# Kernel tuning notes

Hardware: AMD Instinct MI355X
Metric: run time of the kernel (lower is better)

## Reference

```python
import jax, jax.numpy as jnp
import numpy as np

# dims: B batch, T timesteps, S sensors, O obs_dim, E obs_embed_dim, P pe_emb_dim, A inter-sensor attn dim
B, T, S, O, E, P, A, OUT = 64, 128, 64, 4, 64, 16, 10, 128


def positional_encoding(times, pe_dim):
    # standard sinusoidal PE over continuous times -> (B, T, pe_dim)
    # (sin block then cos block; mathematically same frequencies as interleaved torch version)
    freq = jnp.exp(jnp.arange(0, pe_dim, 2, dtype=jnp.float32) * (-jnp.log(10000.0) / pe_dim))
    ang = times[..., None] * freq  # (B, T, pe_dim//2)
    return jnp.concatenate([jnp.sin(ang), jnp.cos(ang)], axis=-1)


def setup_inputs() -> dict:
    key = jax.random.key(0)
    ks = jax.random.split(key, 16)
    x = jax.random.normal(ks[0], (B, T, S, O), dtype=jnp.float32)
    times = jnp.sort(jax.random.uniform(ks[1], (B, T), dtype=jnp.float32) * 100.0, axis=1)
    mask = (jax.random.uniform(ks[2], (B, T, S), dtype=jnp.float32) < 0.8).astype(jnp.float32)
    s = 0.1  # param scale (module inits near zero; use small random for a meaningful baseline)
    params = dict(
        obs_emb_weights=jax.random.normal(ks[3], (S, O, E), dtype=jnp.float32) * s,
        inter_sensor_attn_weights=jax.random.normal(ks[4], (S, A), dtype=jnp.float32) * s,
        W_recv=jax.random.normal(ks[5], (E, A + P), dtype=jnp.float32) * s,
        b_recv=jax.random.normal(ks[6], (A + P,), dtype=jnp.float32) * s,
        bidir_weights=jax.random.normal(ks[7], (S, E), dtype=jnp.float32) * s,
        W_q=jax.random.normal(ks[8], (E + P, A), dtype=jnp.float32) * s,
        b_q=jax.random.normal(ks[9], (A,), dtype=jnp.float32) * s,
        W_k=jax.random.normal(ks[10], (E + P, A), dtype=jnp.float32) * s,
        b_k=jax.random.normal(ks[11], (A,), dtype=jnp.float32) * s,
        W_s=jax.random.normal(ks[12], (T, 1), dtype=jnp.float32) * s,
        b_s=jax.random.normal(ks[13], (1,), dtype=jnp.float32) * s,
        W_emb=jax.random.normal(ks[14], (E + P, OUT), dtype=jnp.float32) * s,
        b_emb=jax.random.normal(ks[15], (OUT,), dtype=jnp.float32) * s,
    )
    return dict(x=x, times=times, mask=mask, **params)


def reference(x, times, mask, obs_emb_weights, inter_sensor_attn_weights,
              W_recv, b_recv, bidir_weights, W_q, b_q, W_k, b_k,
              W_s, b_s, W_emb, b_emb):
    b, t, s, _ = x.shape
    e = obs_emb_weights.shape[-1]
    pe_dim = W_recv.shape[1] - inter_sensor_attn_weights.shape[1]

    # per-sensor observation embedding, masked
    h = jax.nn.relu(jnp.einsum('btso,soe->btse', x, obs_emb_weights))
    h = h * mask[..., None]

    pe = positional_encoding(times, pe_dim)                      # (B,T,P)
    pe_rep = jnp.broadcast_to(pe[:, :, None, :], (b, t, s, pe_dim))

    # inter-sensor attention alpha: (B,T,S_recv,S_send)
    attn_cat = jnp.concatenate(
        [jnp.broadcast_to(inter_sensor_attn_weights[None, None], (b, t, s, inter_sensor_attn_weights.shape[1])),
         pe_rep], axis=-1)                                        # (B,T,S,A+P)
    h_map = h @ W_recv + b_recv                                   # (B,T,S,A+P)
    alpha = jax.nn.relu(jnp.einsum('btid,btjd->btij', h_map, attn_cat))

    bidir = bidir_weights @ bidir_weights.T                       # (S,S)

    def propagate(h_in, adj):
        # fused form of: (h.unsqueeze(2) * (bidir*alpha*adj)[...,None]).sum(3)
        w = bidir[None, None] * alpha * adj[:, None]              # (B,T,S,S)
        return jax.nn.relu(jnp.einsum('btij,btje->btie', w, h_in))

    adj1 = jnp.ones((b, s, s), dtype=x.dtype)
    h = propagate(h, adj1)
    adj2 = adj1 * (alpha.sum(axis=1) / mask.sum(axis=1)[..., None])  # (B,S,S)
    h = propagate(h, adj2)

    H = jnp.concatenate([h, pe_rep], axis=-1).transpose(0, 2, 1, 3)  # (B,S,T,E+P)

    # temporal self-attention
    Q = H @ W_q + b_q                                             # (B,S,T,A)
    K = H @ W_k + b_k
    scale = 1.0 / jnp.sqrt(jnp.float32(e + pe_dim))
    beta = jnp.einsum('bsta,bsua->bstu', Q, K) * scale            # (B,S,T,T)
    beta = (beta @ W_s)[..., 0] + b_s[0]                          # (B,S,T)
    beta = jax.nn.softmax(beta, axis=-1)

    out = jnp.einsum('bst,bstd->bsd', beta, H) @ W_emb + b_emb    # (B,S,OUT)
    return out
```

## Files before the change

### kernel.cpp

```cpp
#include <hip/hip_runtime.h>
#include <hip/hip_bf16.h>


typedef unsigned short u16;
typedef unsigned int u32;
typedef __attribute__((ext_vector_type(8))) short short8;
typedef __attribute__((ext_vector_type(4))) float f32x4;

#define OFF_BIDIR 131072
#define OFF_MS    135168
#define OFF_ADJ   139264
#define OFF_BRP   401408
#define OFF_ST    401424
#define BOFF_WRT  1638464u
#define BOFF_CATX 1642560u
#define BOFF_PEH  1644608u
#define BOFF_ADJS 1906752u
#define BOFF_V    2431040u
#define BOFF_HH   3479616u

__device__ __forceinline__ u16 f2bf(float f){
  __hip_bfloat16 h = __float2bfloat16(f);
  union { __hip_bfloat16 h; u16 u; } v; v.h = h; return v.u;
}
__device__ __forceinline__ u32 pk2bf(float lo, float hi){
  __hip_bfloat162 h = __float22bfloat162_rn(float2{lo, hi});
  union { __hip_bfloat162 h; u32 u; } v; v.h = h; return v.u;
}
__device__ __forceinline__ float bf2f(u16 h){
  union { u32 u; float f; } v; v.u = ((u32)h) << 16; return v.f;
}

__global__ void k_pre(const float* __restrict__ times, const float* __restrict__ mask,
                      const float* __restrict__ Wb, const float* __restrict__ Wrecv,
                      const float* __restrict__ brecv, const float* __restrict__ battn,
                      float* __restrict__ ws_f, char* __restrict__ ws_b) {
  __shared__ float peL[32][17];
  __shared__ float wpe[64][17];
  __shared__ float pm[4][64];
  const int blk = blockIdx.x, tid = threadIdx.x;
  u16* wrt  = (u16*)(ws_b + BOFF_WRT);
  u16* catx = (u16*)(ws_b + BOFF_CATX);
  u16* peh  = (u16*)(ws_b + BOFF_PEH);
  u16* vv   = (u16*)(ws_b + BOFF_V);
  float* ST = ws_f + OFF_ST;
  if (blk < 256) {
    #pragma unroll
    for (int r = 0; r < 2; ++r) {
      int id = blk * 512 + r * 256 + tid;
      int bt = id >> 4, k = id & 15;
      float tv = times[bt];
      int kk = k & 7;
      float fr = expf(-(float)kk * 1.1512925465f);
      float ang = tv * fr;
      float v = (k < 8) ? sinf(ang) : cosf(ang);
      peh[id] = f2bf(v);
      peL[r*16 + (tid >> 4)][k] = v;
    }
    #pragma unroll
    for (int q = 0; q < 4; ++q) {
      int idx = q * 256 + tid;
      wpe[idx >> 4][idx & 15] = Wrecv[(idx >> 4)*26 + 10 + (idx & 15)];
    }
    __syncthreads();
    {
      int btl = tid >> 3, e0 = (tid & 7) * 8;
      float acc[8];
      #pragma unroll
      for (int i = 0; i < 8; ++i) acc[i] = 0.f;
      #pragma unroll
      for (int k = 0; k < 16; ++k) {
        float p = peL[btl][k];
        #pragma unroll
        for (int i = 0; i < 8; ++i) acc[i] += wpe[e0 + i][k] * p;
      }
      u32* dst = (u32*)&vv[(blk*32 + btl)*64 + e0];
      #pragma unroll
      for (int p = 0; p < 4; ++p) dst[p] = pk2bf(acc[2*p], acc[2*p+1]);
      if (tid < 32) {
        float s = 0.f;
        #pragma unroll
        for (int k = 0; k < 16; ++k) s += brecv[10 + k] * peL[tid][k];
        ST[blk*32 + tid] = s;
      }
    }
  } else if (blk < 260) {
    float* bidir = ws_f + OFF_BIDIR;
    int q = blk - 256;
    for (int rr = 0; rr < 4; ++rr) {
      int idx = (q*4 + rr) * 256 + tid;
      int i = idx >> 6, j = idx & 63;
      float acc = 0.f;
      for (int e = 0; e < 64; ++e) acc += Wb[i*64+e] * Wb[j*64+e];
      bidir[idx] = acc;
    }
  } else if (blk == 260) {
    for (int r = 0; r < 8; ++r) {
      int idx = r * 256 + tid;
      int d = idx >> 6, e = idx & 63;
      wrt[idx] = (d < 26) ? f2bf(Wrecv[e*26 + d]) : (u16)0;
    }
    if (tid < 16) ws_f[OFF_BRP + tid] = (tid < 10) ? brecv[tid] : 0.f;
    #pragma unroll
    for (int i = 0; i < 4; ++i) {
      int idx = i * 256 + tid;
      int j = idx >> 4, d = idx & 15;
      catx[idx] = (d < 10) ? f2bf(battn[j*10 + d]) : ((d == 10) ? f2bf(1.f) : (u16)0);
    }
  } else {
    int b = blk - 261;
    int i = tid & 63, q = tid >> 6;
    float s = 0.f;
    for (int t = q*32; t < q*32 + 32; ++t) s += mask[(b*128 + t)*64 + i];
    pm[q][i] = s;
    __syncthreads();
    if (tid < 64)
      (ws_f + OFF_MS)[b*64 + tid] =
          1.0f / (pm[0][tid] + pm[1][tid] + pm[2][tid] + pm[3][tid]);
  }
}

__global__ __launch_bounds__(256)
void k_adj(const float* __restrict__ x, const float* __restrict__ mask,
           const float* __restrict__ Wobs, float* __restrict__ ws_f,
           const char* __restrict__ ws_b) {
  __shared__ __align__(16) u16 hA[64][72];
  __shared__ __align__(16) u16 hmA[64][24];

  const int tid = threadIdx.x;
  const int b = blockIdx.y, tc = blockIdx.x;
  const int w = tid >> 6, l = tid & 63, lr = l & 15, lq = l >> 4, kb = lq * 8;
  const u16* wrt  = (const u16*)(ws_b + BOFF_WRT);
  const u16* catx = (const u16*)(ws_b + BOFF_CATX);
  const u16* vv   = (const u16*)(ws_b + BOFF_V);
  const float* brp = ws_f + OFF_BRP;
  const float* ST = ws_f + OFF_ST;
  float* adj = ws_f + OFF_ADJ;

  const short8 z8 = (short8){0,0,0,0,0,0,0,0};
  const bool lowk = (lq < 2);
  short8 w0 = z8, w1 = z8;
  if (lr < 10) {
    const u16* wr = wrt + lr * 64;
    w0 = *(const short8*)&wr[kb];
    w1 = *(const short8*)&wr[32 + kb];
  }
  short8 bc[4];
  #pragma unroll
  for (int n = 0; n < 4; ++n)
    bc[n] = lowk ? *(const short8*)&catx[(16*n + lr)*16 + lq*8] : z8;
  float4 bv = *(const float4*)&brp[lq*4];

  f32x4 asum[4];
  #pragma unroll
  for (int n = 0; n < 4; ++n) asum[n] = (f32x4){0.f,0.f,0.f,0.f};

  const int e4 = tid & 15, sg = tid >> 4;

  for (int tt = 0; tt < 8; ++tt) {
    int t = tc * 8 + tt;
    int base = b * 128 + t;
    short8 av0 = z8, av1 = z8;
    if (lr == 10) {
      av0 = *(const short8*)&vv[base*64 + kb];
      av1 = *(const short8*)&vv[base*64 + 32 + kb];
    }
    float st = ST[base];
    {
      float4 mk4 = *(const float4*)&mask[base*64 + sg*4];
      float mks[4] = {mk4.x, mk4.y, mk4.z, mk4.w};
      #pragma unroll
      for (int si = 0; si < 4; ++si) {
        int s = sg*4 + si;
        float4 xv = *(const float4*)&x[base*256 + s*4];
        float xo[4] = {xv.x, xv.y, xv.z, xv.w};
        float ax = 0.f, ay = 0.f, az = 0.f, aw = 0.f;
        #pragma unroll
        for (int o = 0; o < 4; ++o) {
          float4 wv = *(const float4*)&Wobs[(s*4+o)*64 + e4*4];
          ax += xo[o]*wv.x; ay += xo[o]*wv.y; az += xo[o]*wv.z; aw += xo[o]*wv.w;
        }
        float mk = mks[si];
        uint2 p;
        p.x = pk2bf(fmaxf(ax,0.f)*mk, fmaxf(ay,0.f)*mk);
        p.y = pk2bf(fmaxf(az,0.f)*mk, fmaxf(aw,0.f)*mk);
        *(uint2*)&hA[s][e4*4] = p;
      }
    }
    __syncthreads();
    {
      short8 a0 = (lr < 10) ? w0 : av0;
      short8 a1 = (lr < 10) ? w1 : av1;
      f32x4 acc = (f32x4){0.f,0.f,0.f,0.f};
      short8 b0 = *(const short8*)&hA[16*w + lr][kb];
      short8 b1 = *(const short8*)&hA[16*w + lr][32 + kb];
      acc = __builtin_amdgcn_mfma_f32_16x16x32_bf16(a0, b0, acc, 0, 0, 0);
      acc = __builtin_amdgcn_mfma_f32_16x16x32_bf16(a1, b1, acc, 0, 0, 0);
      uint2 qq;
      qq.x = pk2bf(acc[0]+bv.x, acc[1]+bv.y);
      qq.y = pk2bf(acc[2]+bv.z, acc[3]+bv.w);
      *(uint2*)&hmA[16*w + lr][lq*4] = qq;
    }
    __syncthreads();
    {
      short8 am = lowk ? *(const short8*)&hmA[16*w + lr][lq*8] : z8;
      #pragma unroll
      for (int n = 0; n < 4; ++n) {
        f32x4 z = (f32x4){st, st, st, st};
        z = __builtin_amdgcn_mfma_f32_16x16x32_bf16(am, bc[n], z, 0, 0, 0);
        #pragma unroll
        for (int reg = 0; reg < 4; ++reg) asum[n][reg] += fmaxf(z[reg], 0.f);
      }
    }
    __syncthreads();
  }
  #pragma unroll
  for (int n = 0; n < 4; ++n) {
    #pragma unroll
    for (int reg = 0; reg < 4; ++reg) {
      int i = 16*w + lq*4 + reg, j = 16*n + lr;
      atomicAdd(&adj[((size_t)b << 12) + (i << 6) + j], asum[n][reg]);
    }
  }
}

__global__ __launch_bounds__(256)
void k_scale(const float* __restrict__ ws_f, char* __restrict__ ws_b) {
  const int b = blockIdx.x, tid = threadIdx.x;
  const float* adj = ws_f + OFF_ADJ + (size_t)b * 4096;
  const float* msI = ws_f + OFF_MS + b * 64;
  u16* as_ = (u16*)(ws_b + BOFF_ADJS) + (size_t)b * 4096;
  #pragma unroll
  for (int k = 0; k < 16; ++k) {
    int idx = k * 256 + tid;
    int i = idx >> 6;
    as_[idx] = f2bf(adj[idx] * msI[i]);
  }
}

__global__ __launch_bounds__(256, 4)
void k_main(const float* __restrict__ x, const float* __restrict__ mask,
            const float* __restrict__ Wobs, const float* __restrict__ ws_f,
            const char* __restrict__ ws_b, u16* __restrict__ Hh) {
  __shared__ __align__(16) char smem[36864];
  u16 (*hA)[72]  = (u16 (*)[72])(smem);
  u16 (*hT)[72]  = (u16 (*)[72])(smem + 9216);
  u16 (*wA)[72]  = (u16 (*)[72])(smem + 18432);
  u16 (*hmA)[24] = (u16 (*)[24])(smem + 27648);
  u16 (*adjS)[72]= (u16 (*)[72])(smem + 27648);

  const int tid = threadIdx.x;
  const int t = blockIdx.x, b = blockIdx.y;
  const int w = tid >> 6, l = tid & 63, lr = l & 15, lq = l >> 4, kb = lq * 8;
  const int base = b * 128 + t;
  const u16* wrt  = (const u16*)(ws_b + BOFF_WRT);
  const u16* catx = (const u16*)(ws_b + BOFF_CATX);
  const u16* vv   = (const u16*)(ws_b + BOFF_V);
  const float* bidirG = ws_f + OFF_BIDIR;
  const float* brp = ws_f + OFF_BRP;
  const int i0 = 16*w + lq*4;
  const short8 z8 = (short8){0,0,0,0,0,0,0,0};
  const bool lowk = (lq < 2);

  const uint4* ag = (const uint4*)(ws_b + BOFF_ADJS + (size_t)b * 8192);
  uint4 g0 = ag[2*tid], g1 = ag[2*tid + 1];
  short8 w0 = z8, w1 = z8;
  if (lr < 10) {
    const u16* wr = wrt + lr * 64;
    w0 = *(const short8*)&wr[kb];
    w1 = *(const short8*)&wr[32 + kb];
  }
  short8 av0 = z8, av1 = z8;
  if (lr == 10) {
    av0 = *(const short8*)&vv[base*64 + kb];
    av1 = *(const short8*)&vv[base*64 + 32 + kb];
  }
  short8 bc[4];
  #pragma unroll
  for (int n = 0; n < 4; ++n)
    bc[n] = lowk ? *(const short8*)&catx[(16*n + lr)*16 + lq*8] : z8;
  float4 bv = *(const float4*)&brp[lq*4];
  const float st = (ws_f + OFF_ST)[base];

  {
    const int e4 = tid & 15, sg = tid >> 4;
    float4 mk4 = *(const float4*)&mask[base*64 + sg*4];
    float mks[4] = {mk4.x, mk4.y, mk4.z, mk4.w};
    #pragma unroll
    for (int si = 0; si < 4; ++si) {
      int s = sg*4 + si;
      float4 xv = *(const float4*)&x[base*256 + s*4];
      float xo[4] = {xv.x, xv.y, xv.z, xv.w};
      float ax = 0.f, ay = 0.f, az = 0.f, aw = 0.f;
      #pragma unroll
      for (int o = 0; o < 4; ++o) {
        float4 wv = *(const float4*)&Wobs[(s*4+o)*64 + e4*4];
        ax += xo[o]*wv.x; ay += xo[o]*wv.y; az += xo[o]*wv.z; aw += xo[o]*wv.w;
      }
      float mk = mks[si];
      uint2 p;
      p.x = pk2bf(fmaxf(ax,0.f)*mk, fmaxf(ay,0.f)*mk);
      p.y = pk2bf(fmaxf(az,0.f)*mk, fmaxf(aw,0.f)*mk);
      *(uint2*)&hA[s][e4*4] = p;
    }
  }
  __syncthreads();

  {
    #pragma unroll
    for (int sp = 0; sp < 8; ++sp) {
      int s = w*16 + sp*2;
      *(u32*)&hT[l][s] = (u32)hA[s][l] | ((u32)hA[s+1][l] << 16);
    }
    short8 a0 = (lr < 10) ? w0 : av0;
    short8 a1 = (lr < 10) ? w1 : av1;
    f32x4 acc = (f32x4){0.f,0.f,0.f,0.f};
    short8 b0 = *(const short8*)&hA[16*w + lr][kb];
    short8 b1 = *(const short8*)&hA[16*w + lr][32 + kb];
    acc = __builtin_amdgcn_mfma_f32_16x16x32_bf16(a0, b0, acc, 0, 0, 0);
    acc = __builtin_amdgcn_mfma_f32_16x16x32_bf16(a1, b1, acc, 0, 0, 0);
    uint2 qq;
    qq.x = pk2bf(acc[0]+bv.x, acc[1]+bv.y);
    qq.y = pk2bf(acc[2]+bv.z, acc[3]+bv.w);
    *(uint2*)&hmA[16*w + lr][lq*4] = qq;
  }
  __syncthreads();

  {
    short8 am = lowk ? *(const short8*)&hmA[16*w + lr][lq*8] : z8;
    #pragma unroll
    for (int n = 0; n < 4; ++n) {
      f32x4 z = (f32x4){st, st, st, st};
      z = __builtin_amdgcn_mfma_f32_16x16x32_bf16(am, bc[n], z, 0, 0, 0);
      int j = 16*n + lr;
      #pragma unroll
      for (int reg = 0; reg < 4; ++reg) {
        float w1v = fmaxf(z[reg], 0.f) * bidirG[((i0+reg) << 6) + j];
        wA[i0 + reg][j] = f2bf(w1v);
      }
    }
  }
  __syncthreads();

  {
    int idx0 = 2*tid, idx1 = 2*tid + 1;
    *(uint4*)&adjS[idx0 >> 3][(idx0 & 7) * 8] = g0;
    *(uint4*)&adjS[idx1 >> 3][(idx1 & 7) * 8] = g1;

    short8 aw0 = *(const short8*)&wA[16*w + lr][kb];
    short8 aw1 = *(const short8*)&wA[16*w + lr][32 + kb];
    #pragma unroll
    for (int n = 0; n < 4; ++n) {
      f32x4 acc = (f32x4){0.f,0.f,0.f,0.f};
      short8 b0 = *(const short8*)&hT[16*n + lr][kb];
      short8 b1 = *(const short8*)&hT[16*n + lr][32 + kb];
      acc = __builtin_amdgcn_mfma_f32_16x16x32_bf16(aw0, b0, acc, 0, 0, 0);
      acc = __builtin_amdgcn_mfma_f32_16x16x32_bf16(aw1, b1, acc, 0, 0, 0);
      int e = 16*n + lr;
      uint2 pp;
      pp.x = pk2bf(fmaxf(acc[0],0.f), fmaxf(acc[1],0.f));
      pp.y = pk2bf(fmaxf(acc[2],0.f), fmaxf(acc[3],0.f));
      *(uint2*)&hA[e][i0] = pp;
    }
  }
  __syncthreads();

  {
    int row = 16*w + lr;
    union { short8 v; u16 h[8]; u32 u[4]; } uw0, uw1, ud0, ud1, oa, ob;
    uw0.v = *(const short8*)&wA[row][kb];
    uw1.v = *(const short8*)&wA[row][32 + kb];
    ud0.v = *(const short8*)&adjS[row][kb];
    ud1.v = *(const short8*)&adjS[row][32 + kb];
    #pragma unroll
    for (int k = 0; k < 4; ++k) {
      oa.u[k] = pk2bf(bf2f(uw0.h[2*k])*bf2f(ud0.h[2*k]),
                      bf2f(uw0.h[2*k+1])*bf2f(ud0.h[2*k+1]));
      ob.u[k] = pk2bf(bf2f(uw1.h[2*k])*bf2f(ud1.h[2*k]),
                      bf2f(uw1.h[2*k+1])*bf2f(ud1.h[2*k+1]));
    }
    short8 a20 = oa.v, a21 = ob.v;
    size_t obase = ((size_t)b * 64) * 8192 + (size_t)t * 64;
    #pragma unroll
    for (int n = 0; n < 4; ++n) {
      f32x4 acc = (f32x4){0.f,0.f,0.f,0.f};
      short8 b0 = *(const short8*)&hA[16*n + lr][kb];
      short8 b1 = *(const short8*)&hA[16*n + lr][32 + kb];
      acc = __builtin_amdgcn_mfma_f32_16x16x32_bf16(a20, b0, acc, 0, 0, 0);
      acc = __builtin_amdgcn_mfma_f32_16x16x32_bf16(a21, b1, acc, 0, 0, 0);
      int e = 16*n + lr;
      u32 p0 = pk2bf(fmaxf(acc[0],0.f), fmaxf(acc[1],0.f));
      u32 p1 = pk2bf(fmaxf(acc[2],0.f), fmaxf(acc[3],0.f));
      Hh[obase + (size_t)(i0+0) * 8192 + e] = (u16)p0;
      Hh[obase + (size_t)(i0+1) * 8192 + e] = (u16)(p0 >> 16);
      Hh[obase + (size_t)(i0+2) * 8192 + e] = (u16)p1;
      Hh[obase + (size_t)(i0+3) * 8192 + e] = (u16)(p1 >> 16);
    }
  }
}

#define HTP 82

__global__ __launch_bounds__(512)
void k_attn(const char* __restrict__ ws_b, const u16* __restrict__ Hh,
            const float* __restrict__ Wq, const float* __restrict__ bq,
            const float* __restrict__ Wk, const float* __restrict__ bk,
            const float* __restrict__ Ws, const float* __restrict__ bs,
            const float* __restrict__ Wemb, const float* __restrict__ bemb,
            float* __restrict__ out) {
  __shared__ u16 Ht[128][HTP];
  __shared__ u16 peB[128][18];
  __shared__ float wsL[128];
  __shared__ float pA[6][80];
  __shared__ float pK[8][10];
  __shared__ float qvL[80];
  __shared__ float pC[4][128];
  __shared__ float bb[128];
  __shared__ float red[4];
  __shared__ float cstL, sWL;

  const int tid = threadIdx.x;
  const int s = blockIdx.x, b = blockIdx.y;
  const float scale = 0.111803398875f;
  const u16* peh = (const u16*)(ws_b + BOFF_PEH);

  const u16* src = Hh + ((size_t)b * 64 + s) * 8192;
  #pragma unroll
  for (int r = 0; r < 2; ++r) {
    int id = r * 512 + tid;
    int tt = id >> 3, c = (id & 7) * 8;
    uint4 q = *(const uint4*)&src[tt * 64 + c];
    u32* dst = (u32*)&Ht[tt][c];
    dst[0] = q.x; dst[1] = q.y; dst[2] = q.z; dst[3] = q.w;
  }
  #pragma unroll
  for (int r = 0; r < 2; ++r) {
    int id = r * 512 + tid;
    u32 pv = ((const u32*)(peh + (size_t)b * 2048))[id];
    *(u32*)&peB[id >> 3][(id & 7) * 2] = pv;
  }
  if (tid < 128) wsL[tid] = Ws[tid];
  __syncthreads();

  if (tid < 480) {
    int d = tid % 80, c = tid / 80;
    int t0 = c * 22, t1 = (t0 + 22 > 128) ? 128 : t0 + 22;
    float a0 = 0.f, a1 = 0.f, a2 = 0.f, a3 = 0.f;
    int t = t0;
    if (d < 64) {
      for (; t + 4 <= t1; t += 4) {
        a0 += wsL[t]   * bf2f(Ht[t][d]);
        a1 += wsL[t+1] * bf2f(Ht[t+1][d]);
        a2 += wsL[t+2] * bf2f(Ht[t+2][d]);
        a3 += wsL[t+3] * bf2f(Ht[t+3][d]);
      }
      for (; t < t1; ++t) a0 += wsL[t] * bf2f(Ht[t][d]);
    } else {
      int k = d - 64;
      for (; t + 4 <= t1; t += 4) {
        a0 += wsL[t]   * bf2f(peB[t][k]);
        a1 += wsL[t+1] * bf2f(peB[t+1][k]);
        a2 += wsL[t+2] * bf2f(peB[t+2][k]);
        a3 += wsL[t+3] * bf2f(peB[t+3][k]);
      }
      for (; t < t1; ++t) a0 += wsL[t] * bf2f(peB[t][k]);
    }
    pA[c][d] = (a0 + a1) + (a2 + a3);
  } else if (tid == 480) {
    float a0 = 0.f, a1 = 0.f, a2 = 0.f, a3 = 0.f;
    for (int t = 0; t < 128; t += 4) {
      a0 += wsL[t]; a1 += wsL[t+1]; a2 += wsL[t+2]; a3 += wsL[t+3];
    }
    sWL = (a0 + a1) + (a2 + a3);
  }
  __syncthreads();

  if (tid < 80) {
    int a = tid % 10, c = tid / 10;
    float a0 = 0.f, a1 = 0.f;
    #pragma unroll
    for (int i = 0; i < 10; i += 2) {
      int d = c * 10 + i;
      float h0 = pA[0][d] + pA[1][d] + pA[2][d] + pA[3][d] + pA[4][d] + pA[5][d];
      float h1 = pA[0][d+1] + pA[1][d+1] + pA[2][d+1] + pA[3][d+1] + pA[4][d+1] + pA[5][d+1];
      a0 += h0 * Wk[d * 10 + a];
      a1 += h1 * Wk[(d+1) * 10 + a];
    }
    pK[c][a] = a0 + a1;
  }
  __syncthreads();

  if (tid <= 80) {
    float kt[10];
    #pragma unroll
    for (int a = 0; a < 10; ++a) {
      float acc = sWL * bk[a];
      #pragma unroll
      for (int c = 0; c < 8; ++c) acc += pK[c][a];
      kt[a] = acc;
    }
    if (tid < 80) {
      float a0 = 0.f, a1 = 0.f;
      #pragma unroll
      for (int a = 0; a < 10; a += 2) {
        a0 += Wq[tid * 10 + a] * kt[a];
        a1 += Wq[tid * 10 + a + 1] * kt[a + 1];
      }
      qvL[tid] = a0 + a1;
    } else {
      float cq = 0.f;
      #pragma unroll
      for (int a = 0; a < 10; ++a) cq += bq[a] * kt[a];
      cstL = scale * cq + bs[0];
    }
  }
  __syncthreads();

  {
    int t = tid & 127, q = tid >> 7;
    float a0 = 0.f, a1 = 0.f, a2 = 0.f, a3 = 0.f;
    const u32* row = (const u32*)&Ht[t][0];
    if (q == 0) {
      #pragma unroll
      for (int i = 0; i < 10; i += 2) {
        u32 p0 = row[i], p1 = row[i+1];
        a0 += bf2f((u16)p0) * qvL[2*i]   + bf2f((u16)(p0 >> 16)) * qvL[2*i+1];
        a1 += bf2f((u16)p1) * qvL[2*i+2] + bf2f((u16)(p1 >> 16)) * qvL[2*i+3];
      }
    } else if (q == 1) {
      #pragma unroll
      for (int i = 10; i < 20; i += 2) {
        u32 p0 = row[i], p1 = row[i+1];
        a0 += bf2f((u16)p0) * qvL[2*i]   + bf2f((u16)(p0 >> 16)) * qvL[2*i+1];
        a1 += bf2f((u16)p1) * qvL[2*i+2] + bf2f((u16)(p1 >> 16)) * qvL[2*i+3];
      }
    } else if (q == 2) {
      #pragma unroll
      for (int i = 20; i < 32; i += 4) {
        u32 p0 = row[i], p1 = row[i+1], p2 = row[i+2], p3 = row[i+3];
        a0 += bf2f((u16)p0) * qvL[2*i]   + bf2f((u16)(p0 >> 16)) * qvL[2*i+1];
        a1 += bf2f((u16)p1) * qvL[2*i+2] + bf2f((u16)(p1 >> 16)) * qvL[2*i+3];
        a2 += bf2f((u16)p2) * qvL[2*i+4] + bf2f((u16)(p2 >> 16)) * qvL[2*i+5];
        a3 += bf2f((u16)p3) * qvL[2*i+6] + bf2f((u16)(p3 >> 16)) * qvL[2*i+7];
      }
    } else {
      #pragma unroll
      for (int k = 0; k < 16; k += 4) {
        a0 += bf2f(peB[t][k])   * qvL[64 + k];
        a1 += bf2f(peB[t][k+1]) * qvL[65 + k];
        a2 += bf2f(peB[t][k+2]) * qvL[66 + k];
        a3 += bf2f(peB[t][k+3]) * qvL[67 + k];
      }
    }
    pC[q][t] = (a0 + a1) + (a2 + a3);
  }
  __syncthreads();

  if (tid < 128) {
    float v = scale * (pC[0][tid] + pC[1][tid] + pC[2][tid] + pC[3][tid]) + cstL;
    bb[tid] = v;
    float mm = v;
    #pragma unroll
    for (int off = 32; off; off >>= 1) mm = fmaxf(mm, __shfl_xor(mm, off));
    if ((tid & 63) == 0) red[tid >> 6] = mm;
  }
  __syncthreads();
  float mx = fmaxf(red[0], red[1]);
  if (tid < 128) {
    float ev = expf(bb[tid] - mx);
    bb[tid] = ev;
    float ss = ev;
    #pragma unroll
    for (int off = 32; off; off >>= 1) ss += __shfl_xor(ss, off);
    if ((tid & 63) == 0) red[2 + (tid >> 6)] = ss;
  }
  __syncthreads();

  if (tid < 480) {
    int d = tid % 80, c = tid / 80;
    int t0 = c * 22, t1 = (t0 + 22 > 128) ? 128 : t0 + 22;
    float a0 = 0.f, a1 = 0.f, a2 = 0.f, a3 = 0.f;
    int t = t0;
    if (d < 64) {
      for (; t + 4 <= t1; t += 4) {
        a0 += bb[t]   * bf2f(Ht[t][d]);
        a1 += bb[t+1] * bf2f(Ht[t+1][d]);
        a2 += bb[t+2] * bf2f(Ht[t+2][d]);
        a3 += bb[t+3] * bf2f(Ht[t+3][d]);
      }
      for (; t < t1; ++t) a0 += bb[t] * bf2f(Ht[t][d]);
    } else {
      int k = d - 64;
      for (; t + 4 <= t1; t += 4) {
        a0 += bb[t]   * bf2f(peB[t][k]);
        a1 += bb[t+1] * bf2f(peB[t+1][k]);
        a2 += bb[t+2] * bf2f(peB[t+2][k]);
        a3 += bb[t+3] * bf2f(peB[t+3][k]);
      }
      for (; t < t1; ++t) a0 += bb[t] * bf2f(peB[t][k]);
    }
    pA[c][d] = (a0 + a1) + (a2 + a3);
  }
  __syncthreads();

  {
    int o = tid & 127, q = tid >> 7;
    int d0 = q * 20;
    float a0 = 0.f, a1 = 0.f, a2 = 0.f, a3 = 0.f;
    #pragma unroll
    for (int i = 0; i < 20; i += 4) {
      int d = d0 + i;
      float h0 = pA[0][d]   + pA[1][d]   + pA[2][d]   + pA[3][d]   + pA[4][d]   + pA[5][d];
      float h1 = pA[0][d+1] + pA[1][d+1] + pA[2][d+1] + pA[3][d+1] + pA[4][d+1] + pA[5][d+1];
      float h2 = pA[0][d+2] + pA[1][d+2] + pA[2][d+2] + pA[3][d+2] + pA[4][d+2] + pA[5][d+2];
      float h3 = pA[0][d+3] + pA[1][d+3] + pA[2][d+3] + pA[3][d+3] + pA[4][d+3] + pA[5][d+3];
      a0 += h0 * Wemb[d * 128 + o];
      a1 += h1 * Wemb[(d+1) * 128 + o];
      a2 += h2 * Wemb[(d+2) * 128 + o];
      a3 += h3 * Wemb[(d+3) * 128 + o];
    }
    pC[q][o] = (a0 + a1) + (a2 + a3);
  }
  __syncthreads();
  if (tid < 128) {
    float rdenom = 1.0f / (red[2] + red[3]);
    out[(((size_t)b * 64 + s) << 7) + tid] =
        bemb[tid] + (pC[0][tid] + pC[1][tid] + pC[2][tid] + pC[3][tid]) * rdenom;
  }
}

extern "C" void kernel_launch(void* const* d_in, const int* in_sizes, int n_in,
                              void* d_out, int out_size, void* d_ws, size_t ws_size,
                              hipStream_t stream) {
  (void)in_sizes; (void)n_in; (void)out_size; (void)ws_size;
  const float* x     = (const float*)d_in[0];
  const float* times = (const float*)d_in[1];
  const float* mask  = (const float*)d_in[2];
  const float* Wobs  = (const float*)d_in[3];
  const float* Wattn = (const float*)d_in[4];
  const float* Wrecv = (const float*)d_in[5];
  const float* brecv = (const float*)d_in[6];
  const float* Wb    = (const float*)d_in[7];
  const float* Wq    = (const float*)d_in[8];
  const float* bq    = (const float*)d_in[9];
  const float* Wk    = (const float*)d_in[10];
  const float* bk    = (const float*)d_in[11];
  const float* Ws    = (const float*)d_in[12];
  const float* bs    = (const float*)d_in[13];
  const float* Wemb  = (const float*)d_in[14];
  const float* bemb  = (const float*)d_in[15];
  float* out = (float*)d_out;
  float* ws_f = (float*)d_ws;
  char* ws_b = (char*)d_ws;
  u16* Hh = (u16*)(ws_b + BOFF_HH);

  hipMemsetAsync(ws_b + (size_t)OFF_ADJ * 4, 0, (size_t)64 * 64 * 64 * 4, stream);
  k_pre<<<325, 256, 0, stream>>>(times, mask, Wb, Wrecv, brecv, Wattn, ws_f, ws_b);
  k_adj<<<dim3(16, 64), 256, 0, stream>>>(x, mask, Wobs, ws_f, ws_b);
  k_scale<<<64, 256, 0, stream>>>(ws_f, ws_b);
  k_main<<<dim3(128, 64), 256, 0, stream>>>(x, mask, Wobs, ws_f, ws_b, Hh);
  k_attn<<<dim3(64, 64), 512, 0, stream>>>(ws_b, Hh, Wq, bq, Wk, bk, Ws, bs, Wemb, bemb, out);
}
```

Measured before the change: 149.9 us.

## Store h and first-hop weights from k_adj instead of recomputing in k_main

k_adj now writes the transposed masked observation embedding and the bidir-scaled alpha weights to global workspace for every (b,t), and k_main loads them instead of recomputing the embedding, the receiver projection and alpha. This removes a duplicated compute pass and two block barriers in k_main, at the cost of roughly 130 MB of extra global writes and reads. The ADJ memset is also folded into extra k_pre blocks, which saves one launch.

```diff
diff --git a/kernel.cpp b/kernel.cpp
--- a/kernel.cpp
+++ b/kernel.cpp
@@ -17,7 +17,9 @@
 #define BOFF_PEH  1644608u
 #define BOFF_ADJS 1906752u
 #define BOFF_V    2431040u
-#define BOFF_HH   3479616u
+#define BOFF_W1   3479616u
+#define BOFF_HT   70588480u
+#define BOFF_HH   137697344u
 
 __device__ __forceinline__ u16 f2bf(float f){
   __hip_bfloat16 h = __float2bfloat16(f);
@@ -107,7 +109,7 @@
       int j = idx >> 4, d = idx & 15;
       catx[idx] = (d < 10) ? f2bf(battn[j*10 + d]) : ((d == 10) ? f2bf(1.f) : (u16)0);
     }
-  } else {
+  } else if (blk < 325) {
     int b = blk - 261;
     int i = tid & 63, q = tid >> 6;
     float s = 0.f;
@@ -117,24 +119,32 @@
     if (tid < 64)
       (ws_f + OFF_MS)[b*64 + tid] =
           1.0f / (pm[0][tid] + pm[1][tid] + pm[2][tid] + pm[3][tid]);
+  } else {
+    int zb = blk - 325;
+    float4 z4 = {0.f, 0.f, 0.f, 0.f};
+    float4* dst = (float4*)(ws_f + OFF_ADJ);
+    #pragma unroll
+    for (int r = 0; r < 16; ++r) dst[zb*4096 + r*256 + tid] = z4;
   }
 }
 
 __global__ __launch_bounds__(256)
 void k_adj(const float* __restrict__ x, const float* __restrict__ mask,
            const float* __restrict__ Wobs, float* __restrict__ ws_f,
-           const char* __restrict__ ws_b) {
+           char* __restrict__ ws_b) {
   __shared__ __align__(16) u16 hA[64][72];
   __shared__ __align__(16) u16 hmA[64][24];
 
   const int tid = threadIdx.x;
   const int b = blockIdx.y, tc = blockIdx.x;
   const int w = tid >> 6, l = tid & 63, lr = l & 15, lq = l >> 4, kb = lq * 8;
+  const int i0 = 16*w + lq*4;
   const u16* wrt  = (const u16*)(ws_b + BOFF_WRT);
   const u16* catx = (const u16*)(ws_b + BOFF_CATX);
   const u16* vv   = (const u16*)(ws_b + BOFF_V);
   const float* brp = ws_f + OFF_BRP;
   const float* ST = ws_f + OFF_ST;
+  const float* bidirG = ws_f + OFF_BIDIR;
   float* adj = ws_f + OFF_ADJ;
 
   const short8 z8 = (short8){0,0,0,0,0,0,0,0};
@@ -150,6 +160,12 @@
   for (int n = 0; n < 4; ++n)
     bc[n] = lowk ? *(const short8*)&catx[(16*n + lr)*16 + lq*8] : z8;
   float4 bv = *(const float4*)&brp[lq*4];
+  float bidirR[4][4];
+  #pragma unroll
+  for (int n = 0; n < 4; ++n)
+    #pragma unroll
+    for (int reg = 0; reg < 4; ++reg)
+      bidirR[n][reg] = bidirG[((i0+reg) << 6) + 16*n + lr];
 
   f32x4 asum[4];
   #pragma unroll
@@ -169,6 +185,7 @@
     {
       float4 mk4 = *(const float4*)&mask[base*64 + sg*4];
       float mks[4] = {mk4.x, mk4.y, mk4.z, mk4.w};
+      u16 hv[4][4];
       #pragma unroll
       for (int si = 0; si < 4; ++si) {
         int s = sg*4 + si;
@@ -185,6 +202,16 @@
         p.x = pk2bf(fmaxf(ax,0.f)*mk, fmaxf(ay,0.f)*mk);
         p.y = pk2bf(fmaxf(az,0.f)*mk, fmaxf(aw,0.f)*mk);
         *(uint2*)&hA[s][e4*4] = p;
+        hv[si][0] = (u16)p.x; hv[si][1] = (u16)(p.x >> 16);
+        hv[si][2] = (u16)p.y; hv[si][3] = (u16)(p.y >> 16);
+      }
+      u16* hTg = (u16*)(ws_b + BOFF_HT) + (size_t)base * 4096;
+      #pragma unroll
+      for (int k = 0; k < 4; ++k) {
+        uint2 q;
+        q.x = (u32)hv[0][k] | ((u32)hv[1][k] << 16);
+        q.y = (u32)hv[2][k] | ((u32)hv[3][k] << 16);
+        *(uint2*)&hTg[(e4*4 + k)*64 + sg*4] = q;
       }
     }
     __syncthreads();
@@ -204,13 +231,27 @@
     __syncthreads();
     {
       short8 am = lowk ? *(const short8*)&hmA[16*w + lr][lq*8] : z8;
+      u32 w1u[8];
       #pragma unroll
       for (int n = 0; n < 4; ++n) {
         f32x4 z = (f32x4){st, st, st, st};
         z = __builtin_amdgcn_mfma_f32_16x16x32_bf16(am, bc[n], z, 0, 0, 0);
+        float w1v[4];
         #pragma unroll
-        for (int reg = 0; reg < 4; ++reg) asum[n][reg] += fmaxf(z[reg], 0.f);
-      }
+        for (int reg = 0; reg < 4; ++reg) {
+          float al = fmaxf(z[reg], 0.f);
+          asum[n][reg] += al;
+          w1v[reg] = al * bidirR[n][reg];
+        }
+        w1u[2*n]   = pk2bf(w1v[0], w1v[1]);
+        w1u[2*n+1] = pk2bf(w1v[2], w1v[3]);
+      }
+      u16* w1g = (u16*)(ws_b + BOFF_W1) + (size_t)base * 4096 + tid * 16;
+      uint4 A, B;
+      A.x = w1u[0]; A.y = w1u[1]; A.z = w1u[2]; A.w = w1u[3];
+      B.x = w1u[4]; B.y = w1u[5]; B.z = w1u[6]; B.w = w1u[7];
+      *(uint4*)&w1g[0] = A;
+      *(uint4*)&w1g[8] = B;
     }
     __syncthreads();
   }
@@ -218,7 +259,7 @@
   for (int n = 0; n < 4; ++n) {
     #pragma unroll
     for (int reg = 0; reg < 4; ++reg) {
-      int i = 16*w + lq*4 + reg, j = 16*n + lr;
+      int i = i0 + reg, j = 16*n + lr;
       atomicAdd(&adj[((size_t)b << 12) + (i << 6) + j], asum[n][reg]);
     }
   }
@@ -239,114 +280,46 @@
 }
 
 __global__ __launch_bounds__(256, 4)
-void k_main(const float* __restrict__ x, const float* __restrict__ mask,
-            const float* __restrict__ Wobs, const float* __restrict__ ws_f,
-            const char* __restrict__ ws_b, u16* __restrict__ Hh) {
+void k_main(const float* __restrict__ ws_f, const char* __restrict__ ws_b,
+            u16* __restrict__ Hh) {
   __shared__ __align__(16) char smem[36864];
-  u16 (*hA)[72]  = (u16 (*)[72])(smem);
+  u16 (*h1L)[72] = (u16 (*)[72])(smem);
   u16 (*hT)[72]  = (u16 (*)[72])(smem + 9216);
   u16 (*wA)[72]  = (u16 (*)[72])(smem + 18432);
-  u16 (*hmA)[24] = (u16 (*)[24])(smem + 27648);
   u16 (*adjS)[72]= (u16 (*)[72])(smem + 27648);
 
   const int tid = threadIdx.x;
   const int t = blockIdx.x, b = blockIdx.y;
   const int w = tid >> 6, l = tid & 63, lr = l & 15, lq = l >> 4, kb = lq * 8;
   const int base = b * 128 + t;
-  const u16* wrt  = (const u16*)(ws_b + BOFF_WRT);
-  const u16* catx = (const u16*)(ws_b + BOFF_CATX);
-  const u16* vv   = (const u16*)(ws_b + BOFF_V);
-  const float* bidirG = ws_f + OFF_BIDIR;
-  const float* brp = ws_f + OFF_BRP;
   const int i0 = 16*w + lq*4;
-  const short8 z8 = (short8){0,0,0,0,0,0,0,0};
-  const bool lowk = (lq < 2);
 
   const uint4* ag = (const uint4*)(ws_b + BOFF_ADJS + (size_t)b * 8192);
   uint4 g0 = ag[2*tid], g1 = ag[2*tid + 1];
-  short8 w0 = z8, w1 = z8;
-  if (lr < 10) {
-    const u16* wr = wrt + lr * 64;
-    w0 = *(const short8*)&wr[kb];
-    w1 = *(const short8*)&wr[32 + kb];
-  }
-  short8 av0 = z8, av1 = z8;
-  if (lr == 10) {
-    av0 = *(const short8*)&vv[base*64 + kb];
-    av1 = *(const short8*)&vv[base*64 + 32 + kb];
-  }
-  short8 bc[4];
-  #pragma unroll
-  for (int n = 0; n < 4; ++n)
-    bc[n] = lowk ? *(const short8*)&catx[(16*n + lr)*16 + lq*8] : z8;
-  float4 bv = *(const float4*)&brp[lq*4];
-  const float st = (ws_f + OFF_ST)[base];
+  const uint4* hp = (const uint4*)((const u16*)(ws_b + BOFF_HT) + (size_t)base * 4096);
+  uint4 hv0 = hp[2*tid], hv1 = hp[2*tid + 1];
+  const uint4* wp = (const uint4*)((const u16*)(ws_b + BOFF_W1) + (size_t)base * 4096);
+  uint4 wp0 = wp[2*tid], wp1 = wp[2*tid + 1];
 
   {
-    const int e4 = tid & 15, sg = tid >> 4;
-    float4 mk4 = *(const float4*)&mask[base*64 + sg*4];
-    float mks[4] = {mk4.x, mk4.y, mk4.z, mk4.w};
-    #pragma unroll
-    for (int si = 0; si < 4; ++si) {
-      int s = sg*4 + si;
-      float4 xv = *(const float4*)&x[base*256 + s*4];
-      float xo[4] = {xv.x, xv.y, xv.z, xv.w};
-      float ax = 0.f, ay = 0.f, az = 0.f, aw = 0.f;
-      #pragma unroll
-      for (int o = 0; o < 4; ++o) {
-        float4 wv = *(const float4*)&Wobs[(s*4+o)*64 + e4*4];
-        ax += xo[o]*wv.x; ay += xo[o]*wv.y; az += xo[o]*wv.z; aw += xo[o]*wv.w;
-      }
-      float mk = mks[si];
-      uint2 p;
-      p.x = pk2bf(fmaxf(ax,0.f)*mk, fmaxf(ay,0.f)*mk);
-      p.y = pk2bf(fmaxf(az,0.f)*mk, fmaxf(aw,0.f)*mk);
-      *(uint2*)&hA[s][e4*4] = p;
-    }
-  }
-  __syncthreads();
-
-  {
-    #pragma unroll
-    for (int sp = 0; sp < 8; ++sp) {
-      int s = w*16 + sp*2;
-      *(u32*)&hT[l][s] = (u32)hA[s][l] | ((u32)hA[s+1][l] << 16);
-    }
-    short8 a0 = (lr < 10) ? w0 : av0;
-    short8 a1 = (lr < 10) ? w1 : av1;
-    f32x4 acc = (f32x4){0.f,0.f,0.f,0.f};
-    short8 b0 = *(const short8*)&hA[16*w + lr][kb];
-    short8 b1 = *(const short8*)&hA[16*w + lr][32 + kb];
-    acc = __builtin_amdgcn_mfma_f32_16x16x32_bf16(a0, b0, acc, 0, 0, 0);
-    acc = __builtin_amdgcn_mfma_f32_16x16x32_bf16(a1, b1, acc, 0, 0, 0);
-    uint2 qq;
-    qq.x = pk2bf(acc[0]+bv.x, acc[1]+bv.y);
-    qq.y = pk2bf(acc[2]+bv.z, acc[3]+bv.w);
-    *(uint2*)&hmA[16*w + lr][lq*4] = qq;
-  }
-  __syncthreads();
-
-  {
-    short8 am = lowk ? *(const short8*)&hmA[16*w + lr][lq*8] : z8;
+    int r = tid >> 2, c = (tid & 3) * 16;
+    *(uint4*)&hT[r][c]     = hv0;
+    *(uint4*)&hT[r][c + 8] = hv1;
+    u32 q[8] = {wp0.x, wp0.y, wp0.z, wp0.w, wp1.x, wp1.y, wp1.z, wp1.w};
     #pragma unroll
     for (int n = 0; n < 4; ++n) {
-      f32x4 z = (f32x4){st, st, st, st};
-      z = __builtin_amdgcn_mfma_f32_16x16x32_bf16(am, bc[n], z, 0, 0, 0);
       int j = 16*n + lr;
-      #pragma unroll
-      for (int reg = 0; reg < 4; ++reg) {
-        float w1v = fmaxf(z[reg], 0.f) * bidirG[((i0+reg) << 6) + j];
-        wA[i0 + reg][j] = f2bf(w1v);
-      }
-    }
-  }
-  __syncthreads();
-
-  {
+      u32 lo = q[2*n], hi = q[2*n+1];
+      wA[i0+0][j] = (u16)lo; wA[i0+1][j] = (u16)(lo >> 16);
+      wA[i0+2][j] = (u16)hi; wA[i0+3][j] = (u16)(hi >> 16);
+    }
     int idx0 = 2*tid, idx1 = 2*tid + 1;
     *(uint4*)&adjS[idx0 >> 3][(idx0 & 7) * 8] = g0;
     *(uint4*)&adjS[idx1 >> 3][(idx1 & 7) * 8] = g1;
-
+  }
+  __syncthreads();
+
+  {
     short8 aw0 = *(const short8*)&wA[16*w + lr][kb];
     short8 aw1 = *(const short8*)&wA[16*w + lr][32 + kb];
     #pragma unroll
@@ -360,7 +333,7 @@
       uint2 pp;
       pp.x = pk2bf(fmaxf(acc[0],0.f), fmaxf(acc[1],0.f));
       pp.y = pk2bf(fmaxf(acc[2],0.f), fmaxf(acc[3],0.f));
-      *(uint2*)&hA[e][i0] = pp;
+      *(uint2*)&h1L[e][i0] = pp;
     }
   }
   __syncthreads();
@@ -384,8 +357,8 @@
     #pragma unroll
     for (int n = 0; n < 4; ++n) {
       f32x4 acc = (f32x4){0.f,0.f,0.f,0.f};
-      short8 b0 = *(const short8*)&hA[16*n + lr][kb];
-      short8 b1 = *(const short8*)&hA[16*n + lr][32 + kb];
+      short8 b0 = *(const short8*)&h1L[16*n + lr][kb];
+      short8 b1 = *(const short8*)&h1L[16*n + lr][32 + kb];
       acc = __builtin_amdgcn_mfma_f32_16x16x32_bf16(a20, b0, acc, 0, 0, 0);
       acc = __builtin_amdgcn_mfma_f32_16x16x32_bf16(a21, b1, acc, 0, 0, 0);
       int e = 16*n + lr;
@@ -654,10 +627,9 @@
   char* ws_b = (char*)d_ws;
   u16* Hh = (u16*)(ws_b + BOFF_HH);
 
-  hipMemsetAsync(ws_b + (size_t)OFF_ADJ * 4, 0, (size_t)64 * 64 * 64 * 4, stream);
-  k_pre<<<325, 256, 0, stream>>>(times, mask, Wb, Wrecv, brecv, Wattn, ws_f, ws_b);
+  k_pre<<<341, 256, 0, stream>>>(times, mask, Wb, Wrecv, brecv, Wattn, ws_f, ws_b);
   k_adj<<<dim3(16, 64), 256, 0, stream>>>(x, mask, Wobs, ws_f, ws_b);
   k_scale<<<64, 256, 0, stream>>>(ws_f, ws_b);
-  k_main<<<dim3(128, 64), 256, 0, stream>>>(x, mask, Wobs, ws_f, ws_b, Hh);
+  k_main<<<dim3(128, 64), 256, 0, stream>>>(ws_f, ws_b, Hh);
   k_attn<<<dim3(64, 64), 512, 0, stream>>>(ws_b, Hh, Wq, bq, Wk, bk, Ws, bs, Wemb, bemb, out);
 }
```

Result: faster. 137.0 us (-8.6%).
